# Optimization experiments

Measured on AMD Instinct MI355X. Metric: run time of the kernel, lower is better.

## Reference

```python
import jax, jax.numpy as jnp
import numpy as np

N_FFT = 4096
N_STAGES = 3
N_CHUNKS = 2 ** N_STAGES


def _mod_seq(order):
    mset = [0]
    for o in range(order):
        step = 2 ** o
        mset = [x + d for x in mset for d in (0, step)]
    return mset


def _perm_matrix(N, order):
    m = np.zeros((N, N), dtype=np.float32)
    base = 2 ** order
    k = 0
    for p in _mod_seq(order):
        for j in range(N // base):
            m[j * base + p, k] = 1.0
            k += 1
    return m


def setup_inputs() -> dict:
    key = jax.random.key(0)
    x = jax.random.normal(key, (8, 512, N_FFT), dtype=jnp.float32)
    perm = jnp.asarray(_perm_matrix(N_FFT, N_STAGES))
    return {"x": x, "perm": perm}


def reference(x, perm):
    # y[..., k] = sum_i x[..., i] * perm[i, k]  (dense matmul by one-hot permutation)
    y = jnp.matmul(x, perm)  # [B, T, N_FFT]
    return tuple(jnp.split(y, N_CHUNKS, axis=-1))  # N_CHUNKS arrays of [B, T, N_FFT // N_CHUNKS]
```

## Files before the change

kernel.cpp:

```cpp
#include <hip/hip_runtime.h>


typedef float v4f __attribute__((ext_vector_type(4)));

#define COLS_TOTAL  (8u * 512u * 512u)
#define NGROUPS     (COLS_TOTAL / 4)
#define BLOCK       256
#define GRID        1024
#define NTHREADS    (GRID * BLOCK)

__global__ __launch_bounds__(BLOCK) void
FFTPermuter_2748779070248_kernel(const v4f* __restrict__ x4,
                                 v4f* __restrict__ out4) {
    const int t  = blockIdx.x * BLOCK + threadIdx.x;
    const int g0 = t;
    const int g1 = t + NTHREADS;

    v4f v0[8], v1[8];
#pragma unroll
    for (int m = 0; m < 8; ++m) v0[m] = x4[(size_t)g0 * 8 + m];
#pragma unroll
    for (int m = 0; m < 8; ++m) v1[m] = x4[(size_t)g1 * 8 + m];

    const int ms[8] = {0, 4, 2, 6, 1, 5, 3, 7};

#pragma unroll
    for (int c = 0; c < 8; ++c) {
        const int p  = ms[c];
        const int hi = p >> 2, lo = p & 3;
        const size_t cb = (size_t)c * (COLS_TOTAL / 4);
        v4f o;
        o.x = v0[0 + hi][lo];
        o.y = v0[2 + hi][lo];
        o.z = v0[4 + hi][lo];
        o.w = v0[6 + hi][lo];
        __builtin_nontemporal_store(o, &out4[cb + g0]);
        v4f q;
        q.x = v1[0 + hi][lo];
        q.y = v1[2 + hi][lo];
        q.z = v1[4 + hi][lo];
        q.w = v1[6 + hi][lo];
        __builtin_nontemporal_store(q, &out4[cb + g1]);
    }
}

extern "C" void kernel_launch(void* const* d_in, const int* in_sizes, int n_in,
                              void* d_out, int out_size, void* d_ws, size_t ws_size,
                              hipStream_t stream) {
    const v4f* x4   = (const v4f*)d_in[0];
    v4f*       out4 = (v4f*)d_out;

    FFTPermuter_2748779070248_kernel<<<GRID, BLOCK, 0, stream>>>(x4, out4);
}
```

Before: 153.6 us.

## Remap threads for coalesced vector loads and scalar scatter stores

Changes the thread-to-data mapping so each lane loads one float4 at a time, with consecutive lanes reading consecutive 16-byte vectors. Each lane then writes its four floats with scalar nontemporal stores straight to the output chunks picked by the index's low bits. Previously each thread read 128 contiguous bytes and wrote one float4 per chunk. The grid is doubled and the work per thread is reshaped to fit. The aim is fully coalesced reads, at the cost of four times as many narrower store instructions, each lane's pair going to two chunks.

```diff
diff --git a/kernel.cpp b/kernel.cpp
--- a/kernel.cpp
+++ b/kernel.cpp
@@ -3,52 +3,38 @@
 
 typedef float v4f __attribute__((ext_vector_type(4)));
 
-#define COLS_TOTAL  (8u * 512u * 512u)
-#define NGROUPS     (COLS_TOTAL / 4)
-#define BLOCK       256
-#define GRID        1024
-#define NTHREADS    (GRID * BLOCK)
+#define BLOCK     256
+#define GRID      2048
+#define NTHREADS  (GRID * BLOCK)
+#define KPT       8
 
 __global__ __launch_bounds__(BLOCK) void
 FFTPermuter_2748779070248_kernel(const v4f* __restrict__ x4,
-                                 v4f* __restrict__ out4) {
-    const int t  = blockIdx.x * BLOCK + threadIdx.x;
-    const int g0 = t;
-    const int g1 = t + NTHREADS;
+                                 float* __restrict__ out) {
+    const unsigned t = blockIdx.x * BLOCK + threadIdx.x;
 
-    v4f v0[8], v1[8];
+    v4f v[KPT];
 #pragma unroll
-    for (int m = 0; m < 8; ++m) v0[m] = x4[(size_t)g0 * 8 + m];
-#pragma unroll
-    for (int m = 0; m < 8; ++m) v1[m] = x4[(size_t)g1 * 8 + m];
-
-    const int ms[8] = {0, 4, 2, 6, 1, 5, 3, 7};
+    for (int n = 0; n < KPT; ++n)
+        v[n] = x4[(size_t)t + (size_t)n * NTHREADS];
 
 #pragma unroll
-    for (int c = 0; c < 8; ++c) {
-        const int p  = ms[c];
-        const int hi = p >> 2, lo = p & 3;
-        const size_t cb = (size_t)c * (COLS_TOTAL / 4);
-        v4f o;
-        o.x = v0[0 + hi][lo];
-        o.y = v0[2 + hi][lo];
-        o.z = v0[4 + hi][lo];
-        o.w = v0[6 + hi][lo];
-        __builtin_nontemporal_store(o, &out4[cb + g0]);
-        v4f q;
-        q.x = v1[0 + hi][lo];
-        q.y = v1[2 + hi][lo];
-        q.z = v1[4 + hi][lo];
-        q.w = v1[6 + hi][lo];
-        __builtin_nontemporal_store(q, &out4[cb + g1]);
+    for (int n = 0; n < KPT; ++n) {
+        const unsigned f   = t + (unsigned)n * NTHREADS;
+        const unsigned col = f >> 1;
+        const size_t   lo  = f & 1;
+        __builtin_nontemporal_store(v[n].x, &out[((0 + lo) << 21) + col]);
+        __builtin_nontemporal_store(v[n].y, &out[((4 + lo) << 21) + col]);
+        __builtin_nontemporal_store(v[n].z, &out[((2 + lo) << 21) + col]);
+        __builtin_nontemporal_store(v[n].w, &out[((6 + lo) << 21) + col]);
     }
 }
 
 extern "C" void kernel_launch(void* const* d_in, const int* in_sizes, int n_in,
                               void* d_out, int out_size, void* d_ws, size_t ws_size,
                               hipStream_t stream) {
-    const v4f* x4   = (const v4f*)d_in[0];
-    v4f*       out4 = (v4f*)d_out;
+    const v4f* x4  = (const v4f*)d_in[0];
+    float*     out = (float*)d_out;
 
-    FFTPermuter_2748779070248_kernel<<<GRID, BLOCK, 0, stream>>>(x4, out4);
+    FFTPermuter_2748779070248_kernel<<<GRID, BLOCK, 0, stream>>>(x4, out);
 }
```

After: 155.8 us. No clear change (+1.5%).
